# Kernel tuning notes

Measured on AMD Instinct MI355X. Metric: run time of the kernel, lower is better.

## Reference

```python
import jax, jax.numpy as jnp
import numpy as np

N_NODES = 100000
N_EDGES = 1600000
N_GRAPHS = 2048
HID = 64
IN_F = 14
N_CLS = 2
EPS = 1e-5


def _gcn_conv(x, row, col, w_edge, W, b, n_nodes):
    # PyG GCNConv with add_self_loops=True, normalize=True.
    xw = x @ W  # [N, out]
    # degree on target nodes, self-loop contributes weight 1
    deg = jnp.zeros((n_nodes,), x.dtype).at[col].add(w_edge) + 1.0
    dinv = deg ** -0.5
    norm = dinv[row] * w_edge * dinv[col]  # [E]
    out = jnp.zeros_like(xw).at[col].add(norm[:, None] * xw[row])
    out = out + (dinv * dinv)[:, None] * xw  # self-loop term
    return out + b


def _bn_relu(x, gamma, beta):
    mean = jnp.mean(x, axis=0)
    var = jnp.var(x, axis=0)  # biased, as PyTorch BN training normalization
    y = gamma * (x - mean) * jax.lax.rsqrt(var + EPS) + beta
    return jax.nn.relu(y)


def setup_inputs() -> dict:
    key = jax.random.key(0)
    ks = jax.random.split(key, 8)
    x = jax.random.normal(ks[0], (N_NODES, IN_F), dtype=jnp.float32)
    edge_index = jax.random.randint(ks[1], (2, N_EDGES), 0, N_NODES, dtype=jnp.int64)
    batch = jnp.sort(jax.random.randint(ks[2], (N_NODES,), 0, N_GRAPHS, dtype=jnp.int64))
    edge_weight = jnp.ones((N_EDGES,), dtype=jnp.float32)
    def lin(k, fi, fo):
        s = 1.0 / np.sqrt(fi)
        kw, kb = jax.random.split(k)
        return (jax.random.uniform(kw, (fi, fo), jnp.float32, -s, s),
                jax.random.uniform(kb, (fo,), jnp.float32, -s, s))
    W1, b1 = lin(ks[3], IN_F, HID)
    W2, b2 = lin(ks[4], HID, HID)
    W3, b3 = lin(ks[5], HID, HID)
    fcW, fcb = lin(ks[6], HID, N_CLS)
    g = jnp.ones((HID,), jnp.float32)
    z = jnp.zeros((HID,), jnp.float32)
    return {
        "x": x, "edge_index": edge_index, "batch": batch, "edge_weight": edge_weight,
        "W1": W1, "b1": b1, "W2": W2, "b2": b2, "W3": W3, "b3": b3,
        "g1": g, "bt1": z, "g2": g, "bt2": z, "g3": g, "bt3": z,
        "fcW": fcW, "fcb": fcb,
    }


def reference(x, edge_index, batch, edge_weight, W1, b1, W2, b2, W3, b3,
              g1, bt1, g2, bt2, g3, bt3, fcW, fcb):
    row, col = edge_index[0], edge_index[1]
    n = x.shape[0]
    h = _bn_relu(_gcn_conv(x, row, col, edge_weight, W1, b1, n), g1, bt1)
    h = _bn_relu(_gcn_conv(h, row, col, edge_weight, W2, b2, n), g2, bt2)
    h = _bn_relu(_gcn_conv(h, row, col, edge_weight, W3, b3, n), g3, bt3)
    node_embs = h  # dropout p=0 is identity
    graph_emb = jax.ops.segment_sum(node_embs, batch, num_segments=N_GRAPHS)
    out = graph_emb @ fcW + fcb
    return (out, node_embs, graph_emb)
```

## Files before the change

### kernel.cpp

```cpp
#include <hip/hip_runtime.h>
#include <hip/hip_fp16.h>

#define N_NODES 100000
#define N_EDGES 1600000
#define EMAX2   2000000
#define N_GRAPHS 2048
#define HID 64
#define IN_F 14
#define N_CLS 2
#define EPS 1e-5f

#define BSHIFT 9
#define NBUCK 196
#define ABLOCKS 256
#define CHUNK (N_EDGES / ABLOCKS)

#define NBLK2 128
#define NCHUNK2 ((N_NODES + NBLK2 - 1) / NBLK2)

#define NQUADS 8192

typedef _Float16 half_t;
typedef _Float16 half8 __attribute__((ext_vector_type(8)));
typedef float f32x4 __attribute__((ext_vector_type(4)));

#define GSTRIDE ((size_t)N_NODES * 16)


__global__ __launch_bounds__(256) void histA_kernel(const int* __restrict__ col,
                                                    int* __restrict__ histG,
                                                    float* __restrict__ gemb,
                                                    float* __restrict__ stats3) {
    __shared__ int hl[NBUCK];
    for (int i = threadIdx.x; i < NBUCK; i += 256) hl[i] = 0;
    for (int k = threadIdx.x; k < 512; k += 256)
        gemb[(size_t)blockIdx.x * 512 + k] = 0.f;
    if (blockIdx.x == 0 && threadIdx.x < 384) stats3[threadIdx.x] = 0.f;
    __syncthreads();
    int e0 = blockIdx.x * CHUNK;
    for (int e = e0 + threadIdx.x; e < e0 + CHUNK; e += 256)
        atomicAdd(&hl[col[e] >> BSHIFT], 1);
    __syncthreads();
    for (int i = threadIdx.x; i < NBUCK; i += 256)
        histG[i * ABLOCKS + blockIdx.x] = hl[i];
}

__global__ __launch_bounds__(256) void scanS1_kernel(const int* __restrict__ histG,
                                                     int* __restrict__ bsumA) {
    __shared__ int ls[256];
    ls[threadIdx.x] = histG[blockIdx.x * 256 + threadIdx.x];
    __syncthreads();
    for (int off = 128; off > 0; off >>= 1) {
        if (threadIdx.x < off) ls[threadIdx.x] += ls[threadIdx.x + off];
        __syncthreads();
    }
    if (threadIdx.x == 0) bsumA[blockIdx.x] = ls[0];
}

__global__ __launch_bounds__(256) void scanS3_kernel(int* __restrict__ histG,
                                                     const int* __restrict__ bsumA,
                                                     int* __restrict__ bsumX,
                                                     int* __restrict__ ptr) {
    __shared__ int ls[256], bs[256];
    int t = threadIdx.x;
    int rawB = (blockIdx.x < NBUCK) ? bsumA[blockIdx.x] : 0;
    bs[t] = (t < NBUCK) ? bsumA[t] : 0;
    int idx = blockIdx.x * 256 + t;
    int v = histG[idx];
    ls[t] = v;
    __syncthreads();
    for (int off = 1; off < 256; off <<= 1) {
        int x = ls[t];
        int y = bs[t];
        if (t >= off) { x += ls[t - off]; y += bs[t - off]; }
        __syncthreads();
        ls[t] = x; bs[t] = y;
        __syncthreads();
    }
    int bexcl = bs[blockIdx.x] - rawB;
    histG[idx] = ls[t] - v + bexcl;
    if (t == 0) bsumX[blockIdx.x] = bexcl;
    if (blockIdx.x == 0 && t == 0) ptr[N_NODES] = N_EDGES;
}

__global__ __launch_bounds__(256) void scatterA_kernel(const int* __restrict__ row,
                                                       const int* __restrict__ col,
                                                       const float* __restrict__ w,
                                                       const int* __restrict__ histG,
                                                       int2* __restrict__ EA) {
    __shared__ int cur[NBUCK];
    for (int i = threadIdx.x; i < NBUCK; i += 256)
        cur[i] = histG[i * ABLOCKS + blockIdx.x];
    __syncthreads();
    int e0 = blockIdx.x * CHUNK;
    for (int e = e0 + threadIdx.x; e < e0 + CHUNK; e += 256) {
        int c = col[e];
        int r = row[e];
        int fx = (int)__float2uint_rn(w[e] * 8192.0f);
        int pos = atomicAdd(&cur[c >> BSHIFT], 1);
        EA[pos] = make_int2(r, (fx << 17) | c);
    }
}

__global__ __launch_bounds__(256) void bucketA_kernel(const int2* __restrict__ EA,
                                                      const int* __restrict__ bsumX,
                                                      int* __restrict__ ptr,
                                                      float* __restrict__ dinv) {
    __shared__ int hist[512], wsum[512];
    int b = blockIdx.x;
    int beg = bsumX[b];
    int end = (b == NBUCK - 1) ? N_EDGES : bsumX[b + 1];
    int i0 = threadIdx.x, i1 = threadIdx.x + 256;
    hist[i0] = 0; hist[i1] = 0;
    wsum[i0] = 0; wsum[i1] = 0;
    __syncthreads();
    for (int e = beg + threadIdx.x; e < end; e += 256) {
        int2 ed = EA[e];
        int c9 = ed.y & 511;
        atomicAdd(&hist[c9], 1);
        atomicAdd(&wsum[c9], (int)((unsigned int)ed.y >> 17));
    }
    __syncthreads();
    int cnt0 = hist[i0], cnt1 = hist[i1];
    for (int off = 1; off < 512; off <<= 1) {
        int v0 = hist[i0], v1 = hist[i1];
        int a0 = (i0 >= off) ? hist[i0 - off] : 0;
        int a1 = (i1 >= off) ? hist[i1 - off] : 0;
        __syncthreads();
        hist[i0] = v0 + a0;
        hist[i1] = v1 + a1;
        __syncthreads();
    }
    int excl0 = hist[i0] - cnt0, excl1 = hist[i1] - cnt1;
    int col0 = (b << BSHIFT) + i0, col1 = (b << BSHIFT) + i1;
    if (col0 < N_NODES) {
        ptr[col0] = beg + excl0;
        dinv[col0] = rsqrtf(1.0f + (float)wsum[i0] * (1.0f / 8192.0f));
    }
    if (col1 < N_NODES) {
        ptr[col1] = beg + excl1;
        dinv[col1] = rsqrtf(1.0f + (float)wsum[i1] * (1.0f / 8192.0f));
    }
}


__global__ __launch_bounds__(256) void histD_kernel(const int* __restrict__ ptr,
                                                    int* __restrict__ histD) {
    __shared__ int hl[2048];
    for (int i = threadIdx.x; i < 2048; i += 256) hl[i] = 0;
    __syncthreads();
    int n0 = blockIdx.x * NCHUNK2;
    int n1 = n0 + NCHUNK2; if (n1 > N_NODES) n1 = N_NODES;
    for (int n = n0 + threadIdx.x; n < n1; n += 256) {
        int d = ptr[n + 1] - ptr[n];
        if (d > 255) d = 255;
        atomicAdd(&hl[((threadIdx.x & 7) << 8) + d], 1);
    }
    __syncthreads();
    int s = 0;
#pragma unroll
    for (int c = 0; c < 8; c++) s += hl[(c << 8) + threadIdx.x];
    histD[threadIdx.x * NBLK2 + blockIdx.x] = s;
}

__global__ __launch_bounds__(128) void scanD1_kernel(const int* __restrict__ histD,
                                                     int* __restrict__ rowTot) {
    __shared__ int ls[128];
    ls[threadIdx.x] = histD[blockIdx.x * NBLK2 + threadIdx.x];
    __syncthreads();
    for (int off = 64; off > 0; off >>= 1) {
        if (threadIdx.x < off) ls[threadIdx.x] += ls[threadIdx.x + off];
        __syncthreads();
    }
    if (threadIdx.x == 0) rowTot[blockIdx.x] = ls[0];
}

__global__ __launch_bounds__(128) void scanD3_kernel(int* __restrict__ histD,
                                                     const int* __restrict__ rowTot,
                                                     int* __restrict__ nodeExcl,
                                                     int* __restrict__ edgeExcl,
                                                     int* __restrict__ ptrS) {
    __shared__ int ls[128], sa[256], sb[256];
    int t = threadIdx.x;
    int bin = blockIdx.x;
    int c0 = rowTot[t], c1 = rowTot[t + 128];
    sa[t] = c0;           sa[t + 128] = c1;
    sb[t] = c0 * ((t + 3) & ~3);
    sb[t + 128] = c1 * ((t + 131) & ~3);
    int idx = bin * NBLK2 + t;
    int v = histD[idx];
    ls[t] = v;
    __syncthreads();
    for (int off = 1; off < 256; off <<= 1) {
        int a0 = sa[t], a1 = sa[t + 128];
        int b0 = sb[t], b1 = sb[t + 128];
        int x0 = (t >= off) ? sa[t - off] : 0;
        int x1 = (t + 128 >= off) ? sa[t + 128 - off] : 0;
        int y0 = (t >= off) ? sb[t - off] : 0;
        int y1 = (t + 128 >= off) ? sb[t + 128 - off] : 0;
        __syncthreads();
        sa[t] = a0 + x0; sa[t + 128] = a1 + x1;
        sb[t] = b0 + y0; sb[t + 128] = b1 + y1;
        __syncthreads();
    }
    for (int off = 1; off < 128; off <<= 1) {
        int x = ls[t];
        if (t >= off) x += ls[t - off];
        __syncthreads();
        ls[t] = x;
        __syncthreads();
    }
    int nE = sa[bin] - rowTot[bin];
    histD[idx] = ls[t] - v + nE;
    if (bin == 0) {
        nodeExcl[t] = sa[t] - rowTot[t];
        nodeExcl[t + 128] = sa[t + 128] - rowTot[t + 128];
        edgeExcl[t] = sb[t] - rowTot[t] * ((t + 3) & ~3);
        edgeExcl[t + 128] = sb[t + 128] - rowTot[t + 128] * ((t + 131) & ~3);
        if (t == 127) ptrS[N_NODES] = sb[255];
    }
}

__global__ __launch_bounds__(256) void scatterD_kernel(const int* __restrict__ ptr,
                                                       const int* __restrict__ histD,
                                                       const int* __restrict__ nodeExcl,
                                                       const int* __restrict__ edgeExcl,
                                                       int* __restrict__ perm,
                                                       int* __restrict__ ptrS,
                                                       int* __restrict__ newbase,
                                                       unsigned int* __restrict__ srcoff,
                                                       half_t* __restrict__ normh) {
    __shared__ int cur[256];
    cur[threadIdx.x] = histD[threadIdx.x * NBLK2 + blockIdx.x];
    __syncthreads();
    int n0 = blockIdx.x * NCHUNK2;
    int n1 = n0 + NCHUNK2; if (n1 > N_NODES) n1 = N_NODES;
    for (int n = n0 + threadIdx.x; n < n1; n += 256) {
        int d = ptr[n + 1] - ptr[n];
        if (d > 255) d = 255;
        int dpad = (d + 3) & ~3;
        int pos = atomicAdd(&cur[d], 1);
        int ebase = edgeExcl[d] + (pos - nodeExcl[d]) * dpad;
        perm[pos] = n;
        ptrS[pos] = ebase;
        newbase[n] = ebase;
        for (int k = d; k < dpad; k++) {
            srcoff[ebase + k] = 0u;
            normh[ebase + k] = (half_t)0.f;
        }
    }
}

__global__ __launch_bounds__(256) void qbounds_kernel(const int* __restrict__ ptrS,
                                                      int* __restrict__ qlo) {
    int q = blockIdx.x * 256 + threadIdx.x;
    if (q > NQUADS) return;
    if (q == NQUADS) { qlo[q] = N_NODES; return; }
    long long W = (long long)ptrS[N_NODES] + 8LL * N_NODES;
    long long target = (W * q) / NQUADS;
    int lo = 0, hi = N_NODES;
    while (lo < hi) {
        int mid = (lo + hi) >> 1;
        long long f = (long long)ptrS[mid] + 8LL * mid;
        if (f < target) lo = mid + 1; else hi = mid;
    }
    qlo[q] = lo & ~1;
}

__global__ __launch_bounds__(256) void bucketB_kernel(const int2* __restrict__ EA,
                                                      const int* __restrict__ bsumX,
                                                      const int* __restrict__ newbase,
                                                      unsigned int* __restrict__ srcoff,
                                                      half_t* __restrict__ normh) {
    __shared__ int cur[512];
    int b = blockIdx.x;
    int beg = bsumX[b];
    int end = (b == NBUCK - 1) ? N_EDGES : bsumX[b + 1];
    int i0 = threadIdx.x, i1 = threadIdx.x + 256;
    int col0 = (b << BSHIFT) + i0, col1 = (b << BSHIFT) + i1;
    cur[i0] = (col0 < N_NODES) ? newbase[col0] : 0;
    cur[i1] = (col1 < N_NODES) ? newbase[col1] : 0;
    __syncthreads();
    for (int e = beg + threadIdx.x; e < end; e += 256) {
        int2 ed = EA[e];
        int c = ed.y & 0x1ffff;
        float w = (float)((unsigned int)ed.y >> 17) * (1.0f / 8192.0f);
        int pos = atomicAdd(&cur[c & 511], 1);
        srcoff[pos] = (unsigned int)ed.x << 5;
        normh[pos] = (half_t)w;
    }
}


template <int K>
__global__ __launch_bounds__(256) void gemm_kernel(const float* __restrict__ h,
                                                   const float* __restrict__ W,
                                                   const float* __restrict__ dinv,
                                                   half_t* __restrict__ xw, int n_nodes) {
    int f = threadIdx.x & 63;
    float wcol[K];
#pragma unroll
    for (int k = 0; k < K; k++) wcol[k] = W[k * HID + f];
    half_t* xg = xw + (size_t)(f >> 4) * GSTRIDE + (f & 15);
    int wave = (blockIdx.x * blockDim.x + threadIdx.x) >> 6;
    int nwaves = (gridDim.x * blockDim.x) >> 6;
    for (int n = wave; n < n_nodes; n += nwaves) {
        const float* hr = h + (size_t)n * K;
        float acc = 0.f;
#pragma unroll
        for (int k = 0; k < K; k++) acc += hr[k] * wcol[k];
        xg[(size_t)n * 16] = (half_t)(acc * dinv[n]);
    }
}

__global__ __launch_bounds__(256) void gemm_bn_mfma_kernel(const half_t* __restrict__ h,
                                                           const float* __restrict__ W,
                                                           const float* __restrict__ stats,
                                                           const float* __restrict__ gamma,
                                                           const float* __restrict__ beta,
                                                           const float* __restrict__ dinv,
                                                           half_t* __restrict__ xw, int n_nodes) {
    __shared__ float sc_s[HID], sh_s[HID];
    if (threadIdx.x < 64) {
        float mean = stats[threadIdx.x] * (1.0f / N_NODES);
        float var = stats[64 + threadIdx.x] * (1.0f / N_NODES) - mean * mean;
        float sc = gamma[threadIdx.x] * rsqrtf(var + EPS);
        sc_s[threadIdx.x] = sc;
        sh_s[threadIdx.x] = beta[threadIdx.x] - mean * sc;
    }
    __syncthreads();
    int lane = threadIdx.x & 63;
    int col16 = lane & 15;
    int quad = lane >> 4;

    float scA[2][8], shA[2][8];
#pragma unroll
    for (int kh = 0; kh < 2; kh++)
#pragma unroll
        for (int j = 0; j < 8; j++) {
            int k = kh * 32 + quad * 8 + j;
            scA[kh][j] = sc_s[k];
            shA[kh][j] = sh_s[k];
        }

    half8 bfrag[4][2];
#pragma unroll
    for (int t = 0; t < 4; t++)
#pragma unroll
        for (int kh = 0; kh < 2; kh++)
#pragma unroll
            for (int j = 0; j < 8; j++) {
                int k = kh * 32 + quad * 8 + j;
                bfrag[t][kh][j] = (half_t)W[k * HID + t * 16 + col16];
            }

    int wave = (blockIdx.x * blockDim.x + threadIdx.x) >> 6;
    int nwaves = (gridDim.x * blockDim.x) >> 6;
    int ntiles = n_nodes >> 4;
    for (int tIdx = wave; tIdx < ntiles; tIdx += nwaves) {
        int n0 = tIdx << 4;
        half8 afrag[2];
#pragma unroll
        for (int kh = 0; kh < 2; kh++) {
            int k0 = kh * 32 + quad * 8;
            const half_t* hp = h + (size_t)(k0 >> 4) * GSTRIDE
                                 + (size_t)(n0 + col16) * 16 + (k0 & 15);
            half8 raw = *(const half8*)hp;
#pragma unroll
            for (int j = 0; j < 8; j++) {
                float v = (float)raw[j] * scA[kh][j] + shA[kh][j];
                afrag[kh][j] = (half_t)fmaxf(v, 0.f);
            }
        }
        f32x4 acc[4];
#pragma unroll
        for (int t = 0; t < 4; t++) {
            f32x4 z = {0.f, 0.f, 0.f, 0.f};
            acc[t] = __builtin_amdgcn_mfma_f32_16x16x32_f16(afrag[0], bfrag[t][0], z, 0, 0, 0);
            acc[t] = __builtin_amdgcn_mfma_f32_16x16x32_f16(afrag[1], bfrag[t][1], acc[t], 0, 0, 0);
        }
        f32x4 dv = *(const f32x4*)(dinv + n0 + quad * 4);
#pragma unroll
        for (int t = 0; t < 4; t++) {
            half_t* xg = xw + (size_t)t * GSTRIDE;
#pragma unroll
            for (int r = 0; r < 4; r++) {
                int rowi = n0 + quad * 4 + r;
                xg[(size_t)rowi * 16 + col16] = (half_t)(acc[t][r] * dv[r]);
            }
        }
    }
}

__global__ __launch_bounds__(256) void gather_stats_kernel(const int* __restrict__ ptrS,
                                                           const int* __restrict__ perm,
                                                           const unsigned int* __restrict__ srcoff,
                                                           const unsigned int* __restrict__ normu,
                                                           const half_t* __restrict__ xw,
                                                           const float* __restrict__ dinv,
                                                           const float* __restrict__ b,
                                                           half_t* __restrict__ hp,
                                                           float* __restrict__ stats,
                                                           const int* __restrict__ qlo,
                                                           int n_nodes) {
    int g = (blockIdx.x & 7) >> 1;
    int grank = ((blockIdx.x >> 3) << 1) | (blockIdx.x & 1);
    int lane16 = threadIdx.x & 15;
    int quadLocal = threadIdx.x >> 4;
    int quadId = grank * 16 + quadLocal;

    const half_t* xg = xw + (size_t)g * GSTRIDE;
    const char* xgc = (const char*)xg;
    unsigned int loff = (unsigned int)(lane16 * 2);
    half_t* hpg = hp + (size_t)g * GSTRIDE;
    float bf = b[g * 16 + lane16];
    int base = ((threadIdx.x & 63) >> 4) * 16;

    float s = 0.f, s2 = 0.f;

    int lo = qlo[quadId], hi = qlo[quadId + 1];

    int i = lo;
    int nodeA = 0, begA = 0, cA = 0, nodeB = 0, begB = 0, cB = 0;
    int evA = 0, nvA = 0, evB = 0, nvB = 0;
    if (i < hi) {
        nodeA = perm[i];
        nodeB = perm[i + 1];
        begA = ptrS[i];
        begB = ptrS[i + 1];
        cA = begB - begA;
        cB = ptrS[i + 2] - begB;
        evA = (int)srcoff[begA + lane16];
        nvA = (int)normu[(begA >> 1) + lane16];
        evB = (int)srcoff[begB + lane16];
        nvB = (int)normu[(begB >> 1) + lane16];
    }

    while (i < hi) {
        int inext = i + 2;
        int nodeA2 = 0, begA2 = 0, cA2 = 0, nodeB2 = 0, begB2 = 0, cB2 = 0;
        if (inext < hi) {
            nodeA2 = perm[inext];
            nodeB2 = perm[inext + 1];
            begA2 = ptrS[inext];
            begB2 = ptrS[inext + 1];
            cA2 = begB2 - begA2;
            cB2 = ptrS[inext + 2] - begB2;
        }
        float selfA = (float)xg[(size_t)nodeA * 16 + lane16];
        float diA = dinv[nodeA];
        float selfB = (float)xg[(size_t)nodeB * 16 + lane16];
        float diB = dinv[nodeB];

        __half2 aA0 = __float2half2_rn(0.f), aA1 = __float2half2_rn(0.f);
        __half2 aB0 = __float2half2_rn(0.f), aB1 = __float2half2_rn(0.f);

        for (int j0 = 0; j0 < cB; j0 += 16) {
            int mA = cA - j0; mA = (mA < 0) ? 0 : ((mA > 16) ? 16 : mA);
            int mB = cB - j0; mB = (mB > 16) ? 16 : mB;
            int pA = mA >> 1;
            int pB = mB >> 1;
            int evA2 = 0, nvA2 = 0, evB2 = 0, nvB2 = 0;
            int j1 = j0 + 16;
            if (j1 < cA) {
                evA2 = (int)srcoff[begA + j1 + lane16];
                nvA2 = (int)normu[((begA + j1) >> 1) + lane16];
            }
            if (j1 < cB) {
                evB2 = (int)srcoff[begB + j1 + lane16];
                nvB2 = (int)normu[((begB + j1) >> 1) + lane16];
            }
            for (int p = 0; p < pB; p += 2) {
                unsigned int ub0 = (unsigned int)__shfl(evB, base + 2 * p);
                unsigned int ub1 = (unsigned int)__shfl(evB, base + 2 * p + 1);
                unsigned int ub2 = (unsigned int)__shfl(evB, base + 2 * p + 2);
                unsigned int ub3 = (unsigned int)__shfl(evB, base + 2 * p + 3);
                unsigned int nb0 = (unsigned int)__shfl(nvB, base + p);
                unsigned int nb1 = (unsigned int)__shfl(nvB, base + p + 1);
                __half hb0 = *(const __half*)(xgc + (ub0 + loff));
                __half hb1 = *(const __half*)(xgc + (ub1 + loff));
                __half hb2 = *(const __half*)(xgc + (ub2 + loff));
                __half hb3 = *(const __half*)(xgc + (ub3 + loff));
                aB0 = __hfma2(*(__half2*)&nb0, __halves2half2(hb0, hb1), aB0);
                aB1 = __hfma2(*(__half2*)&nb1, __halves2half2(hb2, hb3), aB1);
                if (p < pA) {
                    unsigned int ua0 = (unsigned int)__shfl(evA, base + 2 * p);
                    unsigned int ua1 = (unsigned int)__shfl(evA, base + 2 * p + 1);
                    unsigned int ua2 = (unsigned int)__shfl(evA, base + 2 * p + 2);
                    unsigned int ua3 = (unsigned int)__shfl(evA, base + 2 * p + 3);
                    unsigned int na0 = (unsigned int)__shfl(nvA, base + p);
                    unsigned int na1 = (unsigned int)__shfl(nvA, base + p + 1);
                    __half ha0 = *(const __half*)(xgc + (ua0 + loff));
                    __half ha1 = *(const __half*)(xgc + (ua1 + loff));
                    __half ha2 = *(const __half*)(xgc + (ua2 + loff));
                    __half ha3 = *(const __half*)(xgc + (ua3 + loff));
                    aA0 = __hfma2(*(__half2*)&na0, __halves2half2(ha0, ha1), aA0);
                    aA1 = __hfma2(*(__half2*)&na1, __halves2half2(ha2, ha3), aA1);
                }
            }
            evA = evA2; nvA = nvA2; evB = evB2; nvB = nvB2;
        }
        if (inext < hi) {
            evA = (int)srcoff[begA2 + lane16];
            nvA = (int)normu[(begA2 >> 1) + lane16];
            evB = (int)srcoff[begB2 + lane16];
            nvB = (int)normu[(begB2 >> 1) + lane16];
        }

        float accA = (__low2float(aA0) + __high2float(aA0))
                   + (__low2float(aA1) + __high2float(aA1));
        float vA = diA * (accA + selfA) + bf;
        hpg[(size_t)nodeA * 16 + lane16] = (half_t)vA;
        float accB = (__low2float(aB0) + __high2float(aB0))
                   + (__low2float(aB1) + __high2float(aB1));
        float vB = diB * (accB + selfB) + bf;
        hpg[(size_t)nodeB * 16 + lane16] = (half_t)vB;
        s += vA + vB;
        s2 += vA * vA + vB * vB;

        i = inext;
        nodeA = nodeA2; begA = begA2; cA = cA2;
        nodeB = nodeB2; begB = begB2; cB = cB2;
    }
    __shared__ float ls[256], ls2[256];
    ls[threadIdx.x] = s;
    ls2[threadIdx.x] = s2;
    __syncthreads();
    if (threadIdx.x < 16) {
        float a = 0.f, aa = 0.f;
#pragma unroll
        for (int k = 0; k < 16; k++) {
            a += ls[k * 16 + threadIdx.x];
            aa += ls2[k * 16 + threadIdx.x];
        }
        atomicAdd(&stats[g * 16 + threadIdx.x], a);
        atomicAdd(&stats[64 + g * 16 + threadIdx.x], aa);
    }
}

__global__ __launch_bounds__(256) void bn_relu_seg_kernel(const half_t* __restrict__ hpl,
                                                          float* __restrict__ h3,
                                                          const float* __restrict__ stats,
                                                          const float* __restrict__ gamma,
                                                          const float* __restrict__ beta,
                                                          const int* __restrict__ batch,
                                                          float* __restrict__ gemb,
                                                          int n_nodes) {
    int g = blockIdx.x * blockDim.x + threadIdx.x;
    int f = g & 63;
    int wave = g >> 6;
    int nwaves = (gridDim.x * blockDim.x) >> 6;
    int chunk = (n_nodes + nwaves - 1) / nwaves;
    int n0 = wave * chunk;
    int n1 = n0 + chunk;
    if (n1 > n_nodes) n1 = n_nodes;
    if (n0 >= n_nodes) return;
    float mean = stats[f] * (1.0f / N_NODES);
    float var = stats[64 + f] * (1.0f / N_NODES) - mean * mean;
    float sc = gamma[f] * rsqrtf(var + EPS);
    float sh = beta[f] - mean * sc;
    const half_t* hg = hpl + (size_t)(f >> 4) * GSTRIDE + (f & 15);
    int curg = batch[n0];
    float racc = 0.f;
    for (int n = n0; n < n1; n++) {
        int bg = batch[n];
        if (bg != curg) {
            atomicAdd(&gemb[(size_t)curg * HID + f], racc);
            racc = 0.f;
            curg = bg;
        }
        float v = (float)hg[(size_t)n * 16] * sc + sh;
        v = fmaxf(v, 0.f);
        h3[(size_t)n * HID + f] = v;
        racc += v;
    }
    atomicAdd(&gemb[(size_t)curg * HID + f], racc);
}

__global__ __launch_bounds__(256) void final_kernel(const float* __restrict__ gemb,
                                                    const float* __restrict__ fcW,
                                                    const float* __restrict__ fcb,
                                                    float* __restrict__ out) {
    int g = blockIdx.x * blockDim.x + threadIdx.x;
    if (g >= N_GRAPHS * N_CLS) return;
    int gr = g >> 1, c = g & 1;
    float acc = fcb[c];
#pragma unroll
    for (int k = 0; k < HID; k++) acc += gemb[gr * HID + k] * fcW[k * N_CLS + c];
    out[g] = acc;
}


extern "C" void kernel_launch(void* const* d_in, const int* in_sizes, int n_in,
                              void* d_out, int out_size, void* d_ws, size_t ws_size,
                              hipStream_t stream) {
    const float* x    = (const float*)d_in[0];
    const int*   ei   = (const int*)d_in[1];
    const int*   batch= (const int*)d_in[2];
    const float* ew   = (const float*)d_in[3];
    const float* W1   = (const float*)d_in[4];
    const float* b1   = (const float*)d_in[5];
    const float* W2   = (const float*)d_in[6];
    const float* b2   = (const float*)d_in[7];
    const float* W3   = (const float*)d_in[8];
    const float* b3   = (const float*)d_in[9];
    const float* g1   = (const float*)d_in[10];
    const float* bt1  = (const float*)d_in[11];
    const float* g2   = (const float*)d_in[12];
    const float* bt2  = (const float*)d_in[13];
    const float* g3   = (const float*)d_in[14];
    const float* bt3  = (const float*)d_in[15];
    const float* fcW  = (const float*)d_in[16];
    const float* fcb  = (const float*)d_in[17];

    const int* row = ei;
    const int* col = ei + N_EDGES;

    float* out_head  = (float*)d_out;
    float* node_embs = out_head + N_GRAPHS * N_CLS;
    float* gemb      = node_embs + (size_t)N_NODES * HID;

    char* bse = (char*)d_ws;
    half_t* xwh = (half_t*)bse;
    char* r1 = bse + (size_t)N_NODES * HID * 2;
    int2*   EA  = (int2*)r1;
    half_t* hpl = (half_t*)r1;
    char* r2 = r1 + (size_t)N_NODES * HID * 2;
    unsigned int* srcoff = (unsigned int*)r2;
    half_t* normh = (half_t*)(srcoff + EMAX2);
    char* r3 = r2 + (size_t)EMAX2 * 6;
    float* dinv  = (float*)r3;
    float* stats3 = dinv + N_NODES;
    int*   ptr   = (int*)(stats3 + 384);
    int*   histG = ptr + N_NODES + 1;
    int*   bsumA = histG + NBUCK * ABLOCKS;
    int*   bsumX = bsumA + NBUCK + 4;
    int*   histD = bsumX + NBUCK + 4;
    int*   rowTot = histD + 256 * NBLK2;
    int*   nodeExcl = rowTot + 256;
    int*   edgeExcl = nodeExcl + 256;
    int*   perm   = edgeExcl + 256;
    int*   newbase= perm + N_NODES;
    int*   ptrS   = newbase + N_NODES;
    int*   qlo    = ptrS + N_NODES + 1;

    const int B   = 256;
    const int gGS = 1024;
    const int gGA = 2048;

    histA_kernel<<<ABLOCKS, B, 0, stream>>>(col, histG, gemb, stats3);
    scanS1_kernel<<<NBUCK, B, 0, stream>>>(histG, bsumA);
    scanS3_kernel<<<NBUCK, B, 0, stream>>>(histG, bsumA, bsumX, ptr);
    scatterA_kernel<<<ABLOCKS, B, 0, stream>>>(row, col, ew, histG, EA);
    bucketA_kernel<<<NBUCK, B, 0, stream>>>(EA, bsumX, ptr, dinv);

    histD_kernel<<<NBLK2, B, 0, stream>>>(ptr, histD);
    scanD1_kernel<<<256, 128, 0, stream>>>(histD, rowTot);
    scanD3_kernel<<<256, 128, 0, stream>>>(histD, rowTot, nodeExcl, edgeExcl, ptrS);
    scatterD_kernel<<<NBLK2, B, 0, stream>>>(ptr, histD, nodeExcl, edgeExcl,
                                             perm, ptrS, newbase, srcoff, normh);
    qbounds_kernel<<<(NQUADS + 256) / 256, B, 0, stream>>>(ptrS, qlo);
    bucketB_kernel<<<NBUCK, B, 0, stream>>>(EA, bsumX, newbase, srcoff, normh);

    float* h3 = node_embs;

    gemm_kernel<IN_F><<<gGS, B, 0, stream>>>(x, W1, dinv, xwh, N_NODES);
    gather_stats_kernel<<<gGA, B, 0, stream>>>(ptrS, perm, srcoff,
                                               (const unsigned int*)normh, xwh,
                                               dinv, b1, hpl, stats3, qlo, N_NODES);

    gemm_bn_mfma_kernel<<<gGS, B, 0, stream>>>(hpl, W2, stats3, g1, bt1, dinv, xwh, N_NODES);
    gather_stats_kernel<<<gGA, B, 0, stream>>>(ptrS, perm, srcoff,
                                               (const unsigned int*)normh, xwh,
                                               dinv, b2, hpl, stats3 + 128, qlo, N_NODES);

    gemm_bn_mfma_kernel<<<gGS, B, 0, stream>>>(hpl, W3, stats3 + 128, g2, bt2, dinv, xwh, N_NODES);
    gather_stats_kernel<<<gGA, B, 0, stream>>>(ptrS, perm, srcoff,
                                               (const unsigned int*)normh, xwh,
                                               dinv, b3, hpl, stats3 + 256, qlo, N_NODES);

    bn_relu_seg_kernel<<<gGS, B, 0, stream>>>(hpl, h3, stats3 + 256, g3, bt3,
                                              batch, gemb, N_NODES);

    final_kernel<<<(N_GRAPHS * N_CLS + B - 1) / B, B, 0, stream>>>(gemb, fcW, fcb, out_head);
}
```

Before: 455.7 us.

## Replace edge-balanced quad ranges with strided pair scheduling in gather kernel

Result: faster. 395.8 us (-13.1%).

```diff
diff --git a/kernel.cpp b/kernel.cpp
--- a/kernel.cpp
+++ b/kernel.cpp
@@ -17,8 +17,6 @@
 
 #define NBLK2 128
 #define NCHUNK2 ((N_NODES + NBLK2 - 1) / NBLK2)
-
-#define NQUADS 8192
 
 typedef _Float16 half_t;
 typedef _Float16 half8 __attribute__((ext_vector_type(8)));
@@ -251,22 +249,6 @@
     }
 }
 
-__global__ __launch_bounds__(256) void qbounds_kernel(const int* __restrict__ ptrS,
-                                                      int* __restrict__ qlo) {
-    int q = blockIdx.x * 256 + threadIdx.x;
-    if (q > NQUADS) return;
-    if (q == NQUADS) { qlo[q] = N_NODES; return; }
-    long long W = (long long)ptrS[N_NODES] + 8LL * N_NODES;
-    long long target = (W * q) / NQUADS;
-    int lo = 0, hi = N_NODES;
-    while (lo < hi) {
-        int mid = (lo + hi) >> 1;
-        long long f = (long long)ptrS[mid] + 8LL * mid;
-        if (f < target) lo = mid + 1; else hi = mid;
-    }
-    qlo[q] = lo & ~1;
-}
-
 __global__ __launch_bounds__(256) void bucketB_kernel(const int2* __restrict__ EA,
                                                       const int* __restrict__ bsumX,
                                                       const int* __restrict__ newbase,
@@ -401,13 +383,13 @@
                                                            const float* __restrict__ b,
                                                            half_t* __restrict__ hp,
                                                            float* __restrict__ stats,
-                                                           const int* __restrict__ qlo,
                                                            int n_nodes) {
     int g = (blockIdx.x & 7) >> 1;
     int grank = ((blockIdx.x >> 3) << 1) | (blockIdx.x & 1);
     int lane16 = threadIdx.x & 15;
     int quadLocal = threadIdx.x >> 4;
     int quadId = grank * 16 + quadLocal;
+    int nquads = (gridDim.x >> 2) * 16;
 
     const half_t* xg = xw + (size_t)g * GSTRIDE;
     const char* xgc = (const char*)xg;
@@ -418,34 +400,37 @@
 
     float s = 0.f, s2 = 0.f;
 
-    int lo = qlo[quadId], hi = qlo[quadId + 1];
-
-    int i = lo;
+    int npairs = n_nodes >> 1;
+    int idx = quadId;
     int nodeA = 0, begA = 0, cA = 0, nodeB = 0, begB = 0, cB = 0;
     int evA = 0, nvA = 0, evB = 0, nvB = 0;
-    if (i < hi) {
-        nodeA = perm[i];
-        nodeB = perm[i + 1];
-        begA = ptrS[i];
-        begB = ptrS[i + 1];
+    if (idx < npairs) {
+        int iA = idx * 2;
+        nodeA = perm[iA];
+        nodeB = perm[iA + 1];
+        begA = ptrS[iA];
+        begB = ptrS[iA + 1];
         cA = begB - begA;
-        cB = ptrS[i + 2] - begB;
-        evA = (int)srcoff[begA + lane16];
-        nvA = (int)normu[(begA >> 1) + lane16];
-        evB = (int)srcoff[begB + lane16];
-        nvB = (int)normu[(begB >> 1) + lane16];
-    }
-
-    while (i < hi) {
-        int inext = i + 2;
+        cB = ptrS[iA + 2] - begB;
+        int mA = (cA > 16) ? 16 : cA;
+        int mB = (cB > 16) ? 16 : cB;
+        if (lane16 < mA) evA = (int)srcoff[begA + lane16];
+        if (lane16 < (mA >> 1)) nvA = (int)normu[(begA >> 1) + lane16];
+        if (lane16 < mB) evB = (int)srcoff[begB + lane16];
+        if (lane16 < (mB >> 1)) nvB = (int)normu[(begB >> 1) + lane16];
+    }
+
+    while (idx < npairs) {
+        int inext = idx + nquads;
         int nodeA2 = 0, begA2 = 0, cA2 = 0, nodeB2 = 0, begB2 = 0, cB2 = 0;
-        if (inext < hi) {
-            nodeA2 = perm[inext];
-            nodeB2 = perm[inext + 1];
-            begA2 = ptrS[inext];
-            begB2 = ptrS[inext + 1];
+        if (inext < npairs) {
+            int iN = inext * 2;
+            nodeA2 = perm[iN];
+            nodeB2 = perm[iN + 1];
+            begA2 = ptrS[iN];
+            begB2 = ptrS[iN + 1];
             cA2 = begB2 - begA2;
-            cB2 = ptrS[inext + 2] - begB2;
+            cB2 = ptrS[iN + 2] - begB2;
         }
         float selfA = (float)xg[(size_t)nodeA * 16 + lane16];
         float diA = dinv[nodeA];
@@ -463,12 +448,14 @@
             int evA2 = 0, nvA2 = 0, evB2 = 0, nvB2 = 0;
             int j1 = j0 + 16;
             if (j1 < cA) {
-                evA2 = (int)srcoff[begA + j1 + lane16];
-                nvA2 = (int)normu[((begA + j1) >> 1) + lane16];
+                int m2 = cA - j1; if (m2 > 16) m2 = 16;
+                if (lane16 < m2) evA2 = (int)srcoff[begA + j1 + lane16];
+                if (lane16 < (m2 >> 1)) nvA2 = (int)normu[((begA + j1) >> 1) + lane16];
             }
             if (j1 < cB) {
-                evB2 = (int)srcoff[begB + j1 + lane16];
-                nvB2 = (int)normu[((begB + j1) >> 1) + lane16];
+                int m2 = cB - j1; if (m2 > 16) m2 = 16;
+                if (lane16 < m2) evB2 = (int)srcoff[begB + j1 + lane16];
+                if (lane16 < (m2 >> 1)) nvB2 = (int)normu[((begB + j1) >> 1) + lane16];
             }
             for (int p = 0; p < pB; p += 2) {
                 unsigned int ub0 = (unsigned int)__shfl(evB, base + 2 * p);
@@ -500,11 +487,13 @@
             }
             evA = evA2; nvA = nvA2; evB = evB2; nvB = nvB2;
         }
-        if (inext < hi) {
-            evA = (int)srcoff[begA2 + lane16];
-            nvA = (int)normu[(begA2 >> 1) + lane16];
-            evB = (int)srcoff[begB2 + lane16];
-            nvB = (int)normu[(begB2 >> 1) + lane16];
+        if (inext < npairs) {
+            int mA0 = (cA2 > 16) ? 16 : cA2;
+            int mB0 = (cB2 > 16) ? 16 : cB2;
+            evA = (lane16 < mA0) ? (int)srcoff[begA2 + lane16] : 0;
+            nvA = (lane16 < (mA0 >> 1)) ? (int)normu[(begA2 >> 1) + lane16] : 0;
+            evB = (lane16 < mB0) ? (int)srcoff[begB2 + lane16] : 0;
+            nvB = (lane16 < (mB0 >> 1)) ? (int)normu[(begB2 >> 1) + lane16] : 0;
         }
 
         float accA = (__low2float(aA0) + __high2float(aA0))
@@ -518,7 +507,7 @@
         s += vA + vB;
         s2 += vA * vA + vB * vB;
 
-        i = inext;
+        idx = inext;
         nodeA = nodeA2; begA = begA2; cA = cA2;
         nodeB = nodeB2; begB = begB2; cB = cB2;
     }
@@ -642,7 +631,6 @@
     int*   perm   = edgeExcl + 256;
     int*   newbase= perm + N_NODES;
     int*   ptrS   = newbase + N_NODES;
-    int*   qlo    = ptrS + N_NODES + 1;
 
     const int B   = 256;
     const int gGS = 1024;
@@ -659,7 +647,6 @@
     scanD3_kernel<<<256, 128, 0, stream>>>(histD, rowTot, nodeExcl, edgeExcl, ptrS);
     scatterD_kernel<<<NBLK2, B, 0, stream>>>(ptr, histD, nodeExcl, edgeExcl,
                                              perm, ptrS, newbase, srcoff, normh);
-    qbounds_kernel<<<(NQUADS + 256) / 256, B, 0, stream>>>(ptrS, qlo);
     bucketB_kernel<<<NBUCK, B, 0, stream>>>(EA, bsumX, newbase, srcoff, normh);
 
     float* h3 = node_embs;
@@ -667,17 +654,17 @@
     gemm_kernel<IN_F><<<gGS, B, 0, stream>>>(x, W1, dinv, xwh, N_NODES);
     gather_stats_kernel<<<gGA, B, 0, stream>>>(ptrS, perm, srcoff,
                                                (const unsigned int*)normh, xwh,
-                                               dinv, b1, hpl, stats3, qlo, N_NODES);
+                                               dinv, b1, hpl, stats3, N_NODES);
 
     gemm_bn_mfma_kernel<<<gGS, B, 0, stream>>>(hpl, W2, stats3, g1, bt1, dinv, xwh, N_NODES);
     gather_stats_kernel<<<gGA, B, 0, stream>>>(ptrS, perm, srcoff,
                                                (const unsigned int*)normh, xwh,
-                                               dinv, b2, hpl, stats3 + 128, qlo, N_NODES);
+                                               dinv, b2, hpl, stats3 + 128, N_NODES);
 
     gemm_bn_mfma_kernel<<<gGS, B, 0, stream>>>(hpl, W3, stats3 + 128, g2, bt2, dinv, xwh, N_NODES);
     gather_stats_kernel<<<gGA, B, 0, stream>>>(ptrS, perm, srcoff,
                                                (const unsigned int*)normh, xwh,
-                                               dinv, b3, hpl, stats3 + 256, qlo, N_NODES);
+                                               dinv, b3, hpl, stats3 + 256, N_NODES);
 
     bn_relu_seg_kernel<<<gGS, B, 0, stream>>>(hpl, h3, stats3 + 256, g3, bt3,
                                               batch, gemb, N_NODES);
```
